# Kernel tuning notes

Measured on AMD Instinct MI355X. Metric: run time of the kernel, lower is better.

Reference implementation:

```python
import jax, jax.numpy as jnp
import numpy as np

L2_IDX = np.array([0, 1, 2, 4, 24, 26, 35, 38])
S = 16    # n_scalar_features
H = 32    # hidden multiplicity
NL2 = 9   # number of 2e inputs (8 selected kernels + kernel sum)
B = 131072
NK = 40   # n_kernels


def _w3j_222():
    """Wigner 3j / CG tensor for 2e x 2e -> 2e in the real spherical-harmonic
    basis, Frobenius-normalized (e3nn convention up to an overall sign).
    Computed as the 1-D null space of the infinitesimal equivariance constraint."""
    l = 2
    mv = np.arange(-l, l + 1)
    Jp = np.zeros((5, 5), complex)
    for i, m in enumerate(mv[:-1]):
        Jp[i + 1, i] = np.sqrt(l * (l + 1) - m * (m + 1))
    Jm = Jp.conj().T
    Jx, Jy, Jz = (Jp + Jm) / 2, (Jp - Jm) / 2j, np.diag(mv).astype(complex)
    # complex -> real spherical harmonics change of basis
    Q = np.zeros((5, 5), complex)
    for m in mv:
        i = m + l
        if m < 0:
            Q[i, i] = 1j / np.sqrt(2)
            Q[i, l - m] = -1j * (-1.0) ** m / np.sqrt(2)
        elif m == 0:
            Q[i, i] = 1.0
        else:
            Q[i, l - m] = 1 / np.sqrt(2)
            Q[i, i] = (-1.0) ** m / np.sqrt(2)
    Gs = [np.real(-1j * Q @ J @ Q.conj().T) for J in (Jx, Jy, Jz)]  # real so(3) generators
    I5, I25 = np.eye(5), np.eye(25)
    M = np.concatenate([np.kron(G, I25) + np.kron(I5, np.kron(G, I5)) + np.kron(I25, G)
                        for G in Gs], axis=0)
    c = np.linalg.svd(M)[2][-1].reshape(5, 5, 5)
    c = c / np.linalg.norm(c)
    if c.flat[np.argmax(np.abs(c))] < 0:
        c = -c
    return c.astype(np.float32)


C222 = jnp.asarray(_w3j_222())
INV_SQRT5 = float(1.0 / np.sqrt(5.0))  # CG value for l,l->0 and 0,l->l paths


def setup_inputs() -> dict:
    key = jax.random.key(0)
    ks = jax.random.split(key, 10)
    return {
        "scalars": jax.random.normal(ks[0], (B, S), jnp.float32),
        "kernel_t2s": jax.random.normal(ks[1], (B, NK, 5), jnp.float32),
        "w000": jax.random.normal(ks[2], (S, S, H), jnp.float32),
        "w110": jax.random.normal(ks[3], (NL2, NL2, H), jnp.float32),
        "w011": jax.random.normal(ks[4], (S, NL2, H), jnp.float32),
        "w101": jax.random.normal(ks[5], (NL2, S, H), jnp.float32),
        "w111": jax.random.normal(ks[6], (NL2, NL2, H), jnp.float32),
        "v010": jax.random.normal(ks[7], (H, H), jnp.float32),
        "v100": jax.random.normal(ks[8], (H, H), jnp.float32),
        "v110": jax.random.normal(ks[9], (H, H), jnp.float32),
    }


def reference(scalars, kernel_t2s, w000, w110, w011, w101, w111, v010, v100, v110):
    s = scalars                                                  # (B, S)   0e inputs
    t = jnp.concatenate([kernel_t2s[:, L2_IDX, :],
                         kernel_t2s.sum(axis=1, keepdims=True)], axis=1)  # (B, 9, 5) 2e inputs

    # e3nn path-normalization coefficients (component / element defaults)
    c0 = (1.0 / (S * S + NL2 * NL2 * 5)) ** 0.5   # 0e out: fan-in S*S + 9*9*... -> S^2 + 81
    c0 = (1.0 / (S * S + 81)) ** 0.5
    c2 = (5.0 / (18 * S + 81)) ** 0.5             # 2e out: fan-in 9S + 9S + 81

    # ---- tp1(x, x): hidden = Hx0e + Hx2e ----
    h0 = c0 * (jnp.einsum('uvw,bu,bv->bw', w000, s, s)
               + INV_SQRT5 * jnp.einsum('uvw,bui,bvi->bw', w110, t, t))          # (B, H)
    u1 = jnp.einsum('bui,ijk->bujk', t, C222)                                    # (B,9,5,5)
    u2 = jnp.einsum('bujk,bvj->buvk', u1, t)                                     # (B,9,9,5)
    h2 = c2 * (INV_SQRT5 * jnp.einsum('uvw,bu,bvk->bwk', w011, s, t)
               + INV_SQRT5 * jnp.einsum('uvw,bui,bv->bwi', w101, t, s)
               + jnp.einsum('buvk,uvw->bwk', u2, w111))                          # (B, H, 5)

    # ---- tp2(h, h): 1x2e ----
    d = (5.0 / (3 * H * H)) ** 0.5
    a = jnp.einsum('uv,bvj->buj', v110, h2)       # (B, H, 5)
    b2 = jnp.einsum('bui,buj->bij', h2, a)        # (B, 5, 5)
    out = d * (INV_SQRT5 * (jnp.einsum('uv,bu,bvk->bk', v010, h0, h2)
                            + jnp.einsum('uv,buk,bv->bk', v100, h2, h0))
               + jnp.einsum('bij,ijk->bk', b2, C222))                            # (B, 5)
    return out
```

## Files before the change

### kernel.cpp

```cpp
#include <hip/hip_runtime.h>
#include <cmath>


#define DEVINL static __device__ __forceinline__

typedef _Float16 half2_t __attribute__((ext_vector_type(2)));
typedef _Float16 half8_t __attribute__((ext_vector_type(8)));
typedef float    f32x4_t __attribute__((ext_vector_type(4)));
union H8 { half8_t v; half2_t p[4]; };

#define FW0   0
#define FWC   6144
#define FW111 10752
#define PV110 12800
#define PMR   13888
#define SLABH 14976

__device__ __align__(16) _Float16 g_wsh[SLABH];

struct CPack { float v[32]; };

static constexpr int CIa[32] = {2,2,2,4,2,4,4,4, 2,0,0, 2,1,1, 2,3,3, 4,0,0, 4,1,1, 4,3,3, 0,0,1,1,3,3};
static constexpr int CJa[32] = {2,2,4,2,4,2,4,4, 0,2,0, 1,2,1, 3,2,3, 0,4,0, 1,4,1, 3,4,3, 1,3,0,3,0,1};
static constexpr int CKa[32] = {2,4,2,2,4,4,2,4, 0,0,2, 1,1,2, 3,3,2, 0,0,4, 1,1,4, 3,3,4, 3,1,3,0,1,0};

__host__ __device__ inline void tri_uv(int p, int n, int& u, int& v) {
  int base = 0;
  for (int x = 0; x < n; x++) {
    int c = n - x;
    if (p < base + c) { u = x; v = x + (p - base); return; }
    base += c;
  }
  u = n - 1; v = n - 1;
}

static double h_trE3(const double A[3][3], const double B[3][3], const double C[3][3]) {
  double t = 0.0;
  for (int r = 0; r < 3; r++)
    for (int c = 0; c < 3; c++) {
      double ab = 0.0;
      for (int m = 0; m < 3; m++) ab += A[r][m] * B[m][c];
      t += ab * C[c][r];
    }
  return t;
}
static void computeC(CPack& out) {
  const double s2i = 0.7071067811865475244, s6i = 0.4082482904638630164;
  double E[5][3][3] = {
    {{0, s2i, 0}, {s2i, 0, 0}, {0, 0, 0}},
    {{0, 0, 0}, {0, 0, s2i}, {0, s2i, 0}},
    {{-s6i, 0, 0}, {0, -s6i, 0}, {0, 0, 2.0 * s6i}},
    {{0, 0, s2i}, {0, 0, 0}, {s2i, 0, 0}},
    {{s2i, 0, 0}, {0, -s2i, 0}, {0, 0, 0}}
  };
  double T[125], nrm = 0.0;
  for (int f = 0; f < 125; f++) {
    int i = f / 25, j = (f / 5) % 5, k = f % 5;
    T[f] = h_trE3(E[i], E[j], E[k]) + h_trE3(E[i], E[k], E[j]);
    nrm += T[f] * T[f];
  }
  nrm = std::sqrt(nrm);
  int am = 0; double mx = std::fabs(T[0]);
  for (int q = 1; q < 125; q++) { double v = std::fabs(T[q]); if (v > mx) { mx = v; am = q; } }
  const double scale = ((T[am] < 0.0) ? 1.0 : -1.0) / nrm;
  for (int s = 0; s < 32; s++)
    out.v[s] = (float)(scale * T[(CIa[s] * 5 + CJa[s]) * 5 + CKa[s]]);
}

DEVINL float dot2f(half2_t a, half2_t b, float c) {
#if __has_builtin(__builtin_amdgcn_fdot2)
  return __builtin_amdgcn_fdot2(a, b, c, false);
#else
  return fmaf((float)a[0], (float)b[0], fmaf((float)a[1], (float)b[1], c));
#endif
}
DEVINL half2_t pk2(float a, float b) {
  auto r = __builtin_amdgcn_cvt_pkrtz(a, b);
  half2_t o;
  __builtin_memcpy(&o, &r, sizeof(o));
  return o;
}
DEVINL int h2i(half2_t h) { int i; __builtin_memcpy(&i, &h, 4); return i; }
DEVINL half2_t i2h(int i) { half2_t h; __builtin_memcpy(&h, &i, 4); return h; }
DEVINL f32x4_t mfma16(half8_t a, half8_t b, f32x4_t c) {
  return __builtin_amdgcn_mfma_f32_16x16x32_f16(a, b, c, 0, 0, 0);
}
DEVINL void store4h(_Float16* p, f32x4_t d) {
  int2 v;
  v.x = h2i(pk2(d[0], d[1]));
  v.y = h2i(pk2(d[2], d[3]));
  *(int2*)p = v;
}

DEVINL void bar_lds() {
  asm volatile("s_waitcnt lgkmcnt(0)" ::: "memory");
  __builtin_amdgcn_s_barrier();
  __builtin_amdgcn_sched_barrier(0);
}
DEVINL void fence_lds_wave() {
  asm volatile("s_waitcnt lgkmcnt(0)" ::: "memory");
  __builtin_amdgcn_sched_barrier(0);
}

__global__ void ech_setup(const float* __restrict__ w000, const float* __restrict__ w110,
                          const float* __restrict__ w011, const float* __restrict__ w101,
                          const float* __restrict__ w111, const float* __restrict__ v010,
                          const float* __restrict__ v100, const float* __restrict__ v110) {
  const float c0   = 1.0f / sqrtf(337.0f);
  const float inv5 = 0.44721359549995794f;
  const float c2   = sqrtf(5.0f / 369.0f);
  const float dm   = sqrtf(5.0f / 3072.0f) * inv5;
  int gid = blockIdx.x * blockDim.x + threadIdx.x;
  int gs  = gridDim.x * blockDim.x;

  for (int idx = gid; idx < 6144; idx += gs) {
    int j = idx & 7, L = (idx >> 3) & 63, tk = idx >> 9;
    int mt = tk / 6, ks = tk % 6;
    int w = mt * 16 + (L & 15);
    int p = ks * 32 + (L >> 4) * 8 + j;
    float x = 0.0f;
    if (p < 136) {
      int u, v; tri_uv(p, 16, u, v);
      x = c0 * (w000[(u * 16 + v) * 32 + w] + (u != v ? w000[(v * 16 + u) * 32 + w] : 0.0f));
    } else if (p < 181) {
      int u, v; tri_uv(p - 136, 9, u, v);
      x = c0 * inv5 * (w110[(u * 9 + v) * 32 + w] + (u != v ? w110[(v * 9 + u) * 32 + w] : 0.0f));
    }
    g_wsh[FW0 + idx] = (_Float16)x;
  }
  for (int idx = gid; idx < 4608; idx += gs) {
    int j = idx & 7, L = (idx >> 3) & 31, t = idx >> 8;
    int m = t * 16 + (L & 15);
    int w = m / 9, v = m % 9;
    int u = (L >> 4) * 8 + j;
    g_wsh[FWC + idx] =
        (_Float16)(c2 * inv5 * (w011[(u * 9 + v) * 32 + w] + w101[(v * 16 + u) * 32 + w]));
  }
  for (int idx = gid; idx < 2048; idx += gs) {
    int j = idx & 7, L = (idx >> 3) & 63, t = idx >> 9;
    int mt = t >> 1, ks = t & 1;
    int w = mt * 16 + (L & 15);
    int p = ks * 32 + (L >> 4) * 8 + j;
    float x = 0.0f;
    if (p < 45) { int u, v; tri_uv(p, 9, u, v);
      x = c2 * (w111[(u * 9 + v) * 32 + w] + (u != v ? w111[(v * 9 + u) * 32 + w] : 0.0f)); }
    g_wsh[FW111 + idx] = (_Float16)x;
  }
  for (int idx = gid; idx < 1024; idx += gs) {
    int u = idx >> 5, v = idx & 31;
    g_wsh[PV110 + u * 34 + v] = (_Float16)v110[u * 32 + v];
  }
  for (int idx = gid; idx < 1024; idx += gs) {
    int w = idx >> 5, u = idx & 31;
    g_wsh[PMR + w * 34 + u] = (_Float16)(dm * (v010[u * 32 + w] + v100[w * 32 + u]));
  }
}

#define ESZ 444
#define P5MT 272
#define P5K  544
__global__ void __launch_bounds__(512, 4)
ech_main(const float* __restrict__ sc, const float* __restrict__ t2s,
         float* __restrict__ out, int nGroups, CPack C) {
  __shared__ __align__(16) _Float16 slabh[SLABH];
  __shared__ __align__(16) float scr[16 * ESZ];
  __shared__ __align__(16) _Float16 unionH[5280];
  __shared__ __align__(16) _Float16 cvvH[16 * 288];
  __shared__ __align__(16) _Float16 h0st[16 * 40];
  __shared__ int pairs9[48];
  __shared__ int sspair[68];

  const int tid  = threadIdx.x;
  const int lane = tid & 31;
  const int sub  = tid >> 5;
  const int w    = lane;

  _Float16* p5H  = unionH;
  _Float16* h2Bb = unionH + 2720;

  for (int i = tid; i < SLABH / 8; i += 512)
    ((float4*)slabh)[i] = ((const float4*)g_wsh)[i];
  if (tid < 45) { int u, v; tri_uv(tid, 9, u, v); pairs9[tid] = u | (v << 4); }
  if (tid < 68) {
    int u0, v0, u1, v1;
    tri_uv(2 * tid, 16, u0, v0);
    tri_uv(2 * tid + 1, 16, u1, v1);
    sspair[tid] = u0 | (v0 << 4) | (u1 << 8) | (v1 << 12);
  }

  constexpr int L2R[8] = {0, 1, 2, 4, 24, 26, 35, 38};

  float*     E    = scr + sub * ESZ;
  float*     Araw = E;
  _Float16*  qBe  = (_Float16*)E;
  float*     tb   = E + 200;
  _Float16*  sshh = (_Float16*)(E + 272);
  _Float16*  tthh = (_Float16*)(E + 340);
  _Float16*  thh  = (_Float16*)(E + 368);
  float*     sL   = E + 408;
  int*       spad = (int*)(E + 424);

  if (lane < 11)      tthh[45 + lane] = (_Float16)0.f;
  else if (lane < 16) thh[(lane - 11) * 16 + 9] = (_Float16)0.f;
  if (lane >= 24)     spad[lane - 16] = 0;

  float4 pf0 = {0.f, 0.f, 0.f, 0.f};
  float4 pf1 = {0.f, 0.f, 0.f, 0.f};
  float4 pfs = {0.f, 0.f, 0.f, 0.f};
  if (blockIdx.x < nGroups) {
    const int b0 = blockIdx.x * 16 + sub;
    const float4* src = (const float4*)(t2s + (size_t)b0 * 200);
    pf0 = src[lane];
    if (lane < 18) pf1 = src[lane + 32];
    if (lane < 4)  pfs = ((const float4*)(sc + (size_t)b0 * 16))[lane];
  }
  __syncthreads();

  for (int grp = blockIdx.x; grp < nGroups; grp += gridDim.x) {
    const int b = grp * 16 + sub;

    {
      float4* Av = (float4*)Araw;
      Av[lane] = pf0;
      if (lane < 18) Av[lane + 32] = pf1;
      if (lane < 4) ((float4*)sL)[lane] = pfs;
    }
    {
      const int gnext = grp + gridDim.x;
      if (gnext < nGroups) {
        const int bn = gnext * 16 + sub;
        const float4* srcn = (const float4*)(t2s + (size_t)bn * 200);
        pf0 = srcn[lane];
        if (lane < 18) pf1 = srcn[lane + 32];
        if (lane < 4)  pfs = ((const float4*)(sc + (size_t)bn * 16))[lane];
      }
    }
    if (lane < 8) spad[lane] = h2i(pk2(sL[2 * lane], sL[2 * lane + 1]));

    #pragma unroll
    for (int it = 0; it < 2; it++) {
      int idx = lane + 32 * it;
      if (idx < 40) {
        int r = idx / 5, c = idx % 5;
        float val = Araw[L2R[r] * 5 + c];
        tb[r * 8 + c] = val;
        thh[c * 16 + r] = (_Float16)val;
      }
    }
    {
      int l25 = lane % 25;
      int c2 = l25 / 5, j2 = l25 % 5;
      float acc = 0.f;
      #pragma unroll
      for (int rr = 0; rr < 8; rr++) acc += Araw[(j2 + 5 * rr) * 5 + c2];
      float tot = __shfl(acc, 5 * c2 + 0, 32) + __shfl(acc, 5 * c2 + 1, 32)
                + __shfl(acc, 5 * c2 + 2, 32) + __shfl(acc, 5 * c2 + 3, 32)
                + __shfl(acc, 5 * c2 + 4, 32);
      if (lane < 25 && j2 == 0) { tb[64 + c2] = tot; thh[c2 * 16 + 8] = (_Float16)tot; }
    }

    #pragma unroll
    for (int it = 0; it < 2; it++) {
      int idx = lane + 32 * it;
      if (idx < 45) {
        int pr = pairs9[idx];
        int pu = pr & 15, pv = pr >> 4;
        float4 u4 = *(const float4*)(tb + pu * 8); float u5 = tb[pu * 8 + 4];
        float4 v4 = *(const float4*)(tb + pv * 8); float v5 = tb[pv * 8 + 4];
        float tu[5] = {u4.x, u4.y, u4.z, u4.w, u5};
        float tv[5] = {v4.x, v4.y, v4.z, v4.w, v5};
        float tt = tu[0]*tv[0] + tu[1]*tv[1] + tu[2]*tv[2] + tu[3]*tv[3] + tu[4]*tv[4];
        tthh[idx] = (_Float16)tt;
        float qk[5] = {0, 0, 0, 0, 0};
        #pragma unroll
        for (int s = 0; s < 32; s++)
          qk[CKa[s]] = fmaf(C.v[s], tu[CIa[s]] * tv[CJa[s]], qk[CKa[s]]);
        #pragma unroll
        for (int k = 0; k < 5; k++) qBe[k * 64 + idx] = (_Float16)qk[k];
      } else {
        #pragma unroll
        for (int k = 0; k < 5; k++) qBe[k * 64 + idx] = (_Float16)0.f;
      }
    }

    #pragma unroll
    for (int ii = 0; ii < 3; ii++) {
      int slot = lane + 32 * ii;
      if (slot < 68) {
        int t = sspair[slot];
        int u0 = t & 15, v0 = (t >> 4) & 15, u1 = (t >> 8) & 15, v1 = (t >> 12) & 15;
        *(half2_t*)(sshh + 2 * slot) = pk2(sL[u0] * sL[v0], sL[u1] * sL[v1]);
      }
    }
    bar_lds();

    {
      const int wid = tid >> 6;
      const int L   = tid & 63;
      const int e2  = L & 15;
      const int q2  = L >> 4;
      const _Float16* scrH = (const _Float16*)scr;
      if (wid == 0) {
        f32x4_t a0 = {0.f, 0.f, 0.f, 0.f}, a1 = {0.f, 0.f, 0.f, 0.f};
        const _Float16* fw  = slabh + FW0 + L * 8;
        const _Float16* ssb = scrH + e2 * (2 * ESZ) + 544;
        #pragma unroll
        for (int ks = 0; ks < 6; ks++) {
          half8_t bb = *(const half8_t*)(ssb + ks * 32 + q2 * 8);
          a0 = mfma16(*(const half8_t*)(fw + ks * 512), bb, a0);
          a1 = mfma16(*(const half8_t*)(fw + (6 + ks) * 512), bb, a1);
        }
        store4h(h0st + e2 * 40 + q2 * 4, a0);
        store4h(h0st + e2 * 40 + 16 + q2 * 4, a1);
      } else if (wid <= 2) {
        const _Float16* spb = scrH + e2 * (2 * ESZ) + 848;
        half8_t bb = *(const half8_t*)(spb + q2 * 8);
        const int t0 = (wid - 1) * 9;
        half8_t wz = {0, 0, 0, 0, 0, 0, 0, 0};
        #pragma unroll
        for (int t = 0; t < 9; t++) {
          half8_t wa = (q2 < 2) ? *(const half8_t*)(slabh + FWC + (t0 + t) * 256 + L * 8) : wz;
          f32x4_t z4 = {0.f, 0.f, 0.f, 0.f};
          f32x4_t d = mfma16(wa, bb, z4);
          store4h(cvvH + e2 * 288 + (t0 + t) * 16 + q2 * 4, d);
        }
      } else {
        const int k = wid - 3;
        const _Float16* fw = slabh + FW111 + L * 8;
        const _Float16* qb = scrH + e2 * (2 * ESZ) + k * 64;
        f32x4_t d0 = {0.f, 0.f, 0.f, 0.f}, d1 = {0.f, 0.f, 0.f, 0.f};
        #pragma unroll
        for (int ks = 0; ks < 2; ks++) {
          half8_t bb = *(const half8_t*)(qb + ks * 32 + q2 * 8);
          d0 = mfma16(*(const half8_t*)(fw + ks * 512), bb, d0);
          d1 = mfma16(*(const half8_t*)(fw + (2 + ks) * 512), bb, d1);
        }
        store4h(p5H + k * P5K + e2 * 16 + q2 * 4, d0);
        store4h(p5H + k * P5K + P5MT + e2 * 16 + q2 * 4, d1);
      }
    }
    bar_lds();

    float Cvv[9];
    #pragma unroll
    for (int v = 0; v < 9; v++) Cvv[v] = (float)cvvH[sub * 288 + w * 9 + v];
    half2_t cpk[5] = { pk2(Cvv[0], Cvv[1]), pk2(Cvv[2], Cvv[3]),
                       pk2(Cvv[4], Cvv[5]), pk2(Cvv[6], Cvv[7]), pk2(Cvv[8], 0.f) };
    float h2r[5];
    #pragma unroll
    for (int k = 0; k < 5; k++) {
      H8 d; d.v = *(const half8_t*)(thh + k * 16);
      half2_t d4 = *(const half2_t*)(thh + k * 16 + 8);
      float acc = dot2f(cpk[0], d.p[0], 0.f);
      acc = dot2f(cpk[1], d.p[1], acc);
      acc = dot2f(cpk[2], d.p[2], acc);
      acc = dot2f(cpk[3], d.p[3], acc);
      acc = dot2f(cpk[4], d4, acc);
      h2r[k] = acc + (float)p5H[k * P5K + (w >> 4) * P5MT + sub * 16 + (w & 15)];
    }
    #pragma unroll
    for (int k = 0; k < 5; k++) h2Bb[k * 512 + sub * 32 + w] = (_Float16)h2r[k];
    fence_lds_wave();

    float a5[5];
    #pragma unroll
    for (int j = 0; j < 5; j++) {
      const _Float16* hb = h2Bb + j * 512 + sub * 32;
      float acc = 0.f;
      #pragma unroll
      for (int vp = 0; vp < 16; vp++) {
        half2_t wv = *(const half2_t*)(slabh + PV110 + w * 34 + 2 * vp);
        half2_t hv = *(const half2_t*)(hb + 2 * vp);
        acc = dot2f(wv, hv, acc);
      }
      a5[j] = acc;
    }
    float g = 0.f;
    {
      const _Float16* h0b = h0st + sub * 40;
      #pragma unroll
      for (int up = 0; up < 16; up++) {
        half2_t wm = *(const half2_t*)(slabh + PMR + w * 34 + 2 * up);
        half2_t hh = *(const half2_t*)(h0b + 2 * up);
        g = dot2f(wm, hh, g);
      }
    }

    float yv[5] = {0, 0, 0, 0, 0};
    #pragma unroll
    for (int s = 0; s < 32; s++)
      yv[CKa[s]] = fmaf(C.v[s], h2r[CIa[s]] * a5[CJa[s]], yv[CKa[s]]);

    const float DCONST = sqrtf(5.0f / 3072.0f);
    float z[5];
    #pragma unroll
    for (int k = 0; k < 5; k++) z[k] = fmaf(DCONST, yv[k], g * h2r[k]);

    half2_t z01 = pk2(z[0], z[1]);
    half2_t z23 = pk2(z[2], z[3]);
    float   z4r = z[4];
    #pragma unroll
    for (int st = 1; st <= 16; st <<= 1) {
      z01 = z01 + i2h(__shfl_xor(h2i(z01), st));
      z23 = z23 + i2h(__shfl_xor(h2i(z23), st));
      z4r += __shfl_xor(z4r, st);
    }
    if (lane < 5) {
      float val = (lane == 0) ? (float)z01[0]
                : (lane == 1) ? (float)z01[1]
                : (lane == 2) ? (float)z23[0]
                : (lane == 3) ? (float)z23[1] : z4r;
      out[(size_t)b * 5 + lane] = val;
    }
  }
}

extern "C" void kernel_launch(void* const* d_in, const int* in_sizes, int n_in,
                              void* d_out, int out_size, void* d_ws, size_t ws_size,
                              hipStream_t stream) {
  (void)n_in; (void)out_size; (void)d_ws; (void)ws_size;

  CPack C;
  computeC(C);

  ech_setup<<<64, 256, 0, stream>>>(
      (const float*)d_in[2], (const float*)d_in[3], (const float*)d_in[4],
      (const float*)d_in[5], (const float*)d_in[6], (const float*)d_in[7],
      (const float*)d_in[8], (const float*)d_in[9]);

  const int B = in_sizes[0] / 16;
  const int nGroups = B / 16;

  int grid = 512;
  if (grid > nGroups) grid = nGroups;

  ech_main<<<grid, 512, 0, stream>>>(
      (const float*)d_in[0], (const float*)d_in[1], (float*)d_out, nGroups, C);
}
```

Baseline: 253.6 us.

## Fold v110 and v010/v100 weights into first-stage matrices to skip second-layer contractions

The setup kernel now precomposes v110 with the w011/w101 and w111 weights, and v010+v100 with w000/w110. The main kernel therefore produces a5 and g directly from extra MFMA passes in the first stage, instead of running per-lane dot-product loops over h2 and h0 through LDS. This removes an h2 round-trip through LDS, a wave fence and two 16-step dot loops. In exchange it adds MFMA work, loads the FWC/FWC2 weights straight from global memory rather than LDS, and raises LDS use, with the launch-bounds occupancy hint dropped.

```diff
diff --git a/kernel.cpp b/kernel.cpp
--- a/kernel.cpp
+++ b/kernel.cpp
@@ -9,14 +9,20 @@
 typedef float    f32x4_t __attribute__((ext_vector_type(4)));
 union H8 { half8_t v; half2_t p[4]; };
 
-#define FW0   0
-#define FWC   6144
-#define FW111 10752
-#define PV110 12800
-#define PMR   13888
-#define SLABH 14976
-
-__device__ __align__(16) _Float16 g_wsh[SLABH];
+#define GFWC    0
+#define GFWC2   4608
+#define GSTGG   9216
+#define GFMG    9216
+#define GFW111  15360
+#define GF111B  17408
+#define GWSHH   19456
+
+#define SFMG    0
+#define SFW111  6144
+#define SF111B  8192
+#define SLABH   10240
+
+__device__ __align__(16) _Float16 g_wsh[GWSHH];
 
 struct CPack { float v[32]; };
 
@@ -97,10 +103,6 @@
   __builtin_amdgcn_s_barrier();
   __builtin_amdgcn_sched_barrier(0);
 }
-DEVINL void fence_lds_wave() {
-  asm volatile("s_waitcnt lgkmcnt(0)" ::: "memory");
-  __builtin_amdgcn_sched_barrier(0);
-}
 
 __global__ void ech_setup(const float* __restrict__ w000, const float* __restrict__ w110,
                           const float* __restrict__ w011, const float* __restrict__ w101,
@@ -113,28 +115,46 @@
   int gid = blockIdx.x * blockDim.x + threadIdx.x;
   int gs  = gridDim.x * blockDim.x;
 
-  for (int idx = gid; idx < 6144; idx += gs) {
-    int j = idx & 7, L = (idx >> 3) & 63, tk = idx >> 9;
-    int mt = tk / 6, ks = tk % 6;
-    int w = mt * 16 + (L & 15);
-    int p = ks * 32 + (L >> 4) * 8 + j;
-    float x = 0.0f;
-    if (p < 136) {
-      int u, v; tri_uv(p, 16, u, v);
-      x = c0 * (w000[(u * 16 + v) * 32 + w] + (u != v ? w000[(v * 16 + u) * 32 + w] : 0.0f));
-    } else if (p < 181) {
-      int u, v; tri_uv(p - 136, 9, u, v);
-      x = c0 * inv5 * (w110[(u * 9 + v) * 32 + w] + (u != v ? w110[(v * 9 + u) * 32 + w] : 0.0f));
-    }
-    g_wsh[FW0 + idx] = (_Float16)x;
-  }
   for (int idx = gid; idx < 4608; idx += gs) {
     int j = idx & 7, L = (idx >> 3) & 31, t = idx >> 8;
     int m = t * 16 + (L & 15);
     int w = m / 9, v = m % 9;
     int u = (L >> 4) * 8 + j;
-    g_wsh[FWC + idx] =
+    g_wsh[GFWC + idx] =
         (_Float16)(c2 * inv5 * (w011[(u * 9 + v) * 32 + w] + w101[(v * 16 + u) * 32 + w]));
+  }
+  for (int idx = gid; idx < 4608; idx += gs) {
+    int j = idx & 7, L = (idx >> 3) & 31, t = idx >> 8;
+    int m = t * 16 + (L & 15);
+    int up = m / 9, v = m % 9;
+    int u = (L >> 4) * 8 + j;
+    float acc = 0.f;
+    for (int w = 0; w < 32; w++)
+      acc += v110[up * 32 + w] * (w011[(u * 9 + v) * 32 + w] + w101[(v * 16 + u) * 32 + w]);
+    g_wsh[GFWC2 + idx] = (_Float16)(c2 * inv5 * acc);
+  }
+  for (int idx = gid; idx < 6144; idx += gs) {
+    int j = idx & 7, L = (idx >> 3) & 63, tk = idx >> 9;
+    int mt = tk / 6, ks = tk % 6;
+    int wp = mt * 16 + (L & 15);
+    int p = ks * 32 + (L >> 4) * 8 + j;
+    float acc = 0.f;
+    if (p < 136) {
+      int pu, pv; tri_uv(p, 16, pu, pv);
+      for (int w = 0; w < 32; w++) {
+        float w0c = w000[(pu * 16 + pv) * 32 + w] + (pu != pv ? w000[(pv * 16 + pu) * 32 + w] : 0.f);
+        acc += (v010[w * 32 + wp] + v100[wp * 32 + w]) * w0c;
+      }
+      acc *= c0 * dm;
+    } else if (p < 181) {
+      int pu, pv; tri_uv(p - 136, 9, pu, pv);
+      for (int w = 0; w < 32; w++) {
+        float w1 = w110[(pu * 9 + pv) * 32 + w] + (pu != pv ? w110[(pv * 9 + pu) * 32 + w] : 0.f);
+        acc += (v010[w * 32 + wp] + v100[wp * 32 + w]) * w1;
+      }
+      acc *= c0 * inv5 * dm;
+    }
+    g_wsh[GFMG + idx] = (_Float16)acc;
   }
   for (int idx = gid; idx < 2048; idx += gs) {
     int j = idx & 7, L = (idx >> 3) & 63, t = idx >> 9;
@@ -144,29 +164,37 @@
     float x = 0.0f;
     if (p < 45) { int u, v; tri_uv(p, 9, u, v);
       x = c2 * (w111[(u * 9 + v) * 32 + w] + (u != v ? w111[(v * 9 + u) * 32 + w] : 0.0f)); }
-    g_wsh[FW111 + idx] = (_Float16)x;
-  }
-  for (int idx = gid; idx < 1024; idx += gs) {
-    int u = idx >> 5, v = idx & 31;
-    g_wsh[PV110 + u * 34 + v] = (_Float16)v110[u * 32 + v];
-  }
-  for (int idx = gid; idx < 1024; idx += gs) {
-    int w = idx >> 5, u = idx & 31;
-    g_wsh[PMR + w * 34 + u] = (_Float16)(dm * (v010[u * 32 + w] + v100[w * 32 + u]));
+    g_wsh[GFW111 + idx] = (_Float16)x;
+  }
+  for (int idx = gid; idx < 2048; idx += gs) {
+    int j = idx & 7, L = (idx >> 3) & 63, t = idx >> 9;
+    int mt = t >> 1, ks = t & 1;
+    int wp = mt * 16 + (L & 15);
+    int p = ks * 32 + (L >> 4) * 8 + j;
+    float acc = 0.f;
+    if (p < 45) {
+      int pu, pv; tri_uv(p, 9, pu, pv);
+      for (int w = 0; w < 32; w++)
+        acc += v110[wp * 32 + w] *
+               (w111[(pu * 9 + pv) * 32 + w] + (pu != pv ? w111[(pv * 9 + pu) * 32 + w] : 0.f));
+      acc *= c2;
+    }
+    g_wsh[GF111B + idx] = (_Float16)acc;
   }
 }
 
 #define ESZ 444
 #define P5MT 272
 #define P5K  544
-__global__ void __launch_bounds__(512, 4)
+__global__ void __launch_bounds__(512)
 ech_main(const float* __restrict__ sc, const float* __restrict__ t2s,
          float* __restrict__ out, int nGroups, CPack C) {
   __shared__ __align__(16) _Float16 slabh[SLABH];
   __shared__ __align__(16) float scr[16 * ESZ];
-  __shared__ __align__(16) _Float16 unionH[5280];
+  __shared__ __align__(16) _Float16 unionH[5440];
   __shared__ __align__(16) _Float16 cvvH[16 * 288];
-  __shared__ __align__(16) _Float16 h0st[16 * 40];
+  __shared__ __align__(16) _Float16 cvv2H[16 * 288];
+  __shared__ __align__(16) _Float16 gst[16 * 40];
   __shared__ int pairs9[48];
   __shared__ int sspair[68];
 
@@ -176,10 +204,10 @@
   const int w    = lane;
 
   _Float16* p5H  = unionH;
-  _Float16* h2Bb = unionH + 2720;
+  _Float16* p52H = unionH + 2720;
 
   for (int i = tid; i < SLABH / 8; i += 512)
-    ((float4*)slabh)[i] = ((const float4*)g_wsh)[i];
+    ((float4*)slabh)[i] = ((const float4*)(g_wsh + GSTGG))[i];
   if (tid < 45) { int u, v; tri_uv(tid, 9, u, v); pairs9[tid] = u | (v << 4); }
   if (tid < 68) {
     int u0, v0, u1, v1;
@@ -302,7 +330,7 @@
       const _Float16* scrH = (const _Float16*)scr;
       if (wid == 0) {
         f32x4_t a0 = {0.f, 0.f, 0.f, 0.f}, a1 = {0.f, 0.f, 0.f, 0.f};
-        const _Float16* fw  = slabh + FW0 + L * 8;
+        const _Float16* fw  = slabh + SFMG + L * 8;
         const _Float16* ssb = scrH + e2 * (2 * ESZ) + 544;
         #pragma unroll
         for (int ks = 0; ks < 6; ks++) {
@@ -310,43 +338,61 @@
           a0 = mfma16(*(const half8_t*)(fw + ks * 512), bb, a0);
           a1 = mfma16(*(const half8_t*)(fw + (6 + ks) * 512), bb, a1);
         }
-        store4h(h0st + e2 * 40 + q2 * 4, a0);
-        store4h(h0st + e2 * 40 + 16 + q2 * 4, a1);
-      } else if (wid <= 2) {
+        store4h(gst + e2 * 40 + q2 * 4, a0);
+        store4h(gst + e2 * 40 + 16 + q2 * 4, a1);
+      } else if (wid <= 4) {
         const _Float16* spb = scrH + e2 * (2 * ESZ) + 848;
         half8_t bb = *(const half8_t*)(spb + q2 * 8);
-        const int t0 = (wid - 1) * 9;
+        const int t0 = ((wid - 1) & 1) * 9;
+        const _Float16* gw = g_wsh + ((wid <= 2) ? GFWC : GFWC2);
+        _Float16* dst = (wid <= 2) ? cvvH : cvv2H;
         half8_t wz = {0, 0, 0, 0, 0, 0, 0, 0};
         #pragma unroll
         for (int t = 0; t < 9; t++) {
-          half8_t wa = (q2 < 2) ? *(const half8_t*)(slabh + FWC + (t0 + t) * 256 + L * 8) : wz;
+          half8_t wa = (q2 < 2)
+              ? *(const half8_t*)(gw + (t0 + t) * 256 + (size_t)L * 8) : wz;
           f32x4_t z4 = {0.f, 0.f, 0.f, 0.f};
           f32x4_t d = mfma16(wa, bb, z4);
-          store4h(cvvH + e2 * 288 + (t0 + t) * 16 + q2 * 4, d);
+          store4h(dst + e2 * 288 + (t0 + t) * 16 + q2 * 4, d);
         }
       } else {
-        const int k = wid - 3;
-        const _Float16* fw = slabh + FW111 + L * 8;
-        const _Float16* qb = scrH + e2 * (2 * ESZ) + k * 64;
-        f32x4_t d0 = {0.f, 0.f, 0.f, 0.f}, d1 = {0.f, 0.f, 0.f, 0.f};
-        #pragma unroll
-        for (int ks = 0; ks < 2; ks++) {
-          half8_t bb = *(const half8_t*)(qb + ks * 32 + q2 * 8);
-          d0 = mfma16(*(const half8_t*)(fw + ks * 512), bb, d0);
-          d1 = mfma16(*(const half8_t*)(fw + (2 + ks) * 512), bb, d1);
+        const int base = (wid - 5) * 3;
+        const int cnt  = (wid == 7) ? 4 : 3;
+        #pragma unroll
+        for (int t = 0; t < 4; t++) {
+          if (t < cnt) {
+            const int un = base + t;
+            const int k  = (un < 5) ? un : un - 5;
+            const _Float16* fw = slabh + ((un < 5) ? SFW111 : SF111B) + L * 8;
+            _Float16* dst = (un < 5) ? p5H : p52H;
+            const _Float16* qb = scrH + e2 * (2 * ESZ) + k * 64;
+            f32x4_t d0 = {0.f, 0.f, 0.f, 0.f}, d1 = {0.f, 0.f, 0.f, 0.f};
+            #pragma unroll
+            for (int ks = 0; ks < 2; ks++) {
+              half8_t bb = *(const half8_t*)(qb + ks * 32 + q2 * 8);
+              d0 = mfma16(*(const half8_t*)(fw + ks * 512), bb, d0);
+              d1 = mfma16(*(const half8_t*)(fw + (2 + ks) * 512), bb, d1);
+            }
+            store4h(dst + k * P5K + e2 * 16 + q2 * 4, d0);
+            store4h(dst + k * P5K + P5MT + e2 * 16 + q2 * 4, d1);
+          }
         }
-        store4h(p5H + k * P5K + e2 * 16 + q2 * 4, d0);
-        store4h(p5H + k * P5K + P5MT + e2 * 16 + q2 * 4, d1);
       }
     }
     bar_lds();
 
-    float Cvv[9];
-    #pragma unroll
-    for (int v = 0; v < 9; v++) Cvv[v] = (float)cvvH[sub * 288 + w * 9 + v];
+    float Cvv[9], Cw2[9];
+    #pragma unroll
+    for (int v = 0; v < 9; v++) {
+      Cvv[v] = (float)cvvH[sub * 288 + w * 9 + v];
+      Cw2[v] = (float)cvv2H[sub * 288 + w * 9 + v];
+    }
     half2_t cpk[5] = { pk2(Cvv[0], Cvv[1]), pk2(Cvv[2], Cvv[3]),
                        pk2(Cvv[4], Cvv[5]), pk2(Cvv[6], Cvv[7]), pk2(Cvv[8], 0.f) };
-    float h2r[5];
+    half2_t epk[5] = { pk2(Cw2[0], Cw2[1]), pk2(Cw2[2], Cw2[3]),
+                       pk2(Cw2[4], Cw2[5]), pk2(Cw2[6], Cw2[7]), pk2(Cw2[8], 0.f) };
+    float h2r[5], a5[5];
+    const int pidx = (w >> 4) * P5MT + sub * 16 + (w & 15);
     #pragma unroll
     for (int k = 0; k < 5; k++) {
       H8 d; d.v = *(const half8_t*)(thh + k * 16);
@@ -356,35 +402,15 @@
       acc = dot2f(cpk[2], d.p[2], acc);
       acc = dot2f(cpk[3], d.p[3], acc);
       acc = dot2f(cpk[4], d4, acc);
-      h2r[k] = acc + (float)p5H[k * P5K + (w >> 4) * P5MT + sub * 16 + (w & 15)];
-    }
-    #pragma unroll
-    for (int k = 0; k < 5; k++) h2Bb[k * 512 + sub * 32 + w] = (_Float16)h2r[k];
-    fence_lds_wave();
-
-    float a5[5];
-    #pragma unroll
-    for (int j = 0; j < 5; j++) {
-      const _Float16* hb = h2Bb + j * 512 + sub * 32;
-      float acc = 0.f;
-      #pragma unroll
-      for (int vp = 0; vp < 16; vp++) {
-        half2_t wv = *(const half2_t*)(slabh + PV110 + w * 34 + 2 * vp);
-        half2_t hv = *(const half2_t*)(hb + 2 * vp);
-        acc = dot2f(wv, hv, acc);
-      }
-      a5[j] = acc;
-    }
-    float g = 0.f;
-    {
-      const _Float16* h0b = h0st + sub * 40;
-      #pragma unroll
-      for (int up = 0; up < 16; up++) {
-        half2_t wm = *(const half2_t*)(slabh + PMR + w * 34 + 2 * up);
-        half2_t hh = *(const half2_t*)(h0b + 2 * up);
-        g = dot2f(wm, hh, g);
-      }
-    }
+      h2r[k] = acc + (float)p5H[k * P5K + pidx];
+      float ac2 = dot2f(epk[0], d.p[0], 0.f);
+      ac2 = dot2f(epk[1], d.p[1], ac2);
+      ac2 = dot2f(epk[2], d.p[2], ac2);
+      ac2 = dot2f(epk[3], d.p[3], ac2);
+      ac2 = dot2f(epk[4], d4, ac2);
+      a5[k] = ac2 + (float)p52H[k * P5K + pidx];
+    }
+    float g = (float)gst[sub * 40 + w];
 
     float yv[5] = {0, 0, 0, 0, 0};
     #pragma unroll
```

Result: slower. 269.2 us (+6.1%).
